# Performance work log

Measured on AMD Instinct MI355X. Metric: run time of the kernel, lower is better.

Reference implementation:

```python
import jax, jax.numpy as jnp
import numpy as np

CTX_SIZE = 4096
LAYER = 1
N_EMBD = 1024
HEAD_SIZE = 64
B, T = 4, 4096


def setup_inputs() -> dict:
    key = jax.random.key(0)
    ks = jax.random.split(key, 4)
    s = 1.0 / np.sqrt(N_EMBD)
    return {
        "x": jax.random.normal(ks[0], (B, T, N_EMBD), dtype=jnp.float32),
        "Wq": jax.random.normal(ks[1], (N_EMBD, HEAD_SIZE), dtype=jnp.float32) * s,
        "bq": jnp.zeros((HEAD_SIZE,), dtype=jnp.float32),
        "Wk": jax.random.normal(ks[2], (N_EMBD, HEAD_SIZE), dtype=jnp.float32) * s,
        "bk": jnp.zeros((HEAD_SIZE,), dtype=jnp.float32),
        "Wv": jax.random.normal(ks[3], (N_EMBD, HEAD_SIZE), dtype=jnp.float32) * s,
        "bv": jnp.zeros((HEAD_SIZE,), dtype=jnp.float32),
    }


def reference(x, Wq, bq, Wk, bk, Wv, bv):
    Bx, Tx, C = x.shape
    t = CTX_SIZE // (2 ** LAYER)
    cut = min(Tx, t)  # static: shapes are concrete under jit

    k = x @ Wk + bk                      # [B, T, H]
    q = x[:, -cut:, :] @ Wq + bq         # [B, cut, H] (fade: queries on last cut tokens)
    v = x @ Wv + bv                      # [B, T, H]

    att = jnp.einsum("bqh,bkh->bqk", q, k) * (C ** -0.5)  # [B, cut, T]

    # row i corresponds to absolute query position (T - cut + i); causal: key j <= that pos
    q_pos = jnp.arange(cut) + (Tx - cut)   # [cut]
    k_pos = jnp.arange(Tx)                 # [T]
    mask = k_pos[None, :] <= q_pos[:, None]  # [cut, T], True = keep
    att = jnp.where(mask[None, :, :], att, -jnp.inf)
    att = jax.nn.softmax(att, axis=-1)
    # dropout p=0.0 (eval mode): identity

    out = jnp.einsum("bqk,bkh->bqh", att, v)  # [B, cut, H]
    return out
```

## Files before the change

### kernel.cpp

```cpp
#include <hip/hip_runtime.h>

#define BB 4
#define TT 4096
#define CUT 2048
#define CE 1024
#define HD 64
#define QSC 0.045084220027780106f

typedef unsigned short u16;
typedef unsigned int u32;
typedef __attribute__((ext_vector_type(8))) short bf16x8;
typedef __attribute__((ext_vector_type(4))) float f32x4;

__device__ __forceinline__ u16 f2b(float f) {
  union { float f; unsigned u; } v; v.f = f;
  unsigned r = v.u + 0x7fffu + ((v.u >> 16) & 1u);
  return (u16)(r >> 16);
}

__device__ __forceinline__ u32 cvtpk(float lo, float hi) {
  u32 r;
  asm("v_cvt_pk_bf16_f32 %0, %1, %2" : "=v"(r) : "v"(lo), "v"(hi));
  return r;
}

__global__ void wtrans_k(const float* __restrict__ Wk, const float* __restrict__ Wv,
                         const float* __restrict__ Wq, u16* __restrict__ w3f) {
  int id = blockIdx.x * 256 + threadIdx.x;
  int j    = id & 7;
  int lane = (id >> 3) & 63;
  int f    = id >> 9;
  int kstep = f & 31;
  int mnt   = f >> 5;
  int m  = mnt >> 2;
  int nt = mnt & 3;
  int k   = kstep * 32 + (lane >> 4) * 8 + j;
  int col = nt * 16 + (lane & 15);
  const float* W = (m == 0) ? Wk : (m == 1) ? Wv : Wq;
  w3f[id] = f2b(W[k * 64 + col]);
}

__launch_bounds__(256, 2)
__global__ void proj_k(const float* __restrict__ x, const u16* __restrict__ w3f,
                       const float* __restrict__ bk, const float* __restrict__ bv,
                       const float* __restrict__ bq,
                       u16* __restrict__ KF, u16* __restrict__ VF, u16* __restrict__ Qb) {
  __shared__ f32x4 cl[2][2][12][64];
  const int tid  = threadIdx.x;
  const int lane = tid & 63;
  const int kh   = tid >> 6;
  const int l15  = lane & 15;
  const int g    = lane >> 4;
  const int r0   = blockIdx.x * 32;

  f32x4 acc[2][12];
  #pragma unroll
  for (int h = 0; h < 2; ++h)
    #pragma unroll
    for (int t = 0; t < 12; ++t) acc[h][t] = (f32x4){0.f, 0.f, 0.f, 0.f};

  const float* x0 = x + (size_t)(r0 + l15) * CE;
  const float* x1 = x + (size_t)(r0 + 16 + l15) * CE;

  f32x4 xs[2][4];
  {
    const int ko = kh * 256 + g * 8;
    xs[0][0] = *(const f32x4*)(x0 + ko);
    xs[0][1] = *(const f32x4*)(x0 + ko + 4);
    xs[0][2] = *(const f32x4*)(x1 + ko);
    xs[0][3] = *(const f32x4*)(x1 + ko + 4);
  }

  #pragma unroll
  for (int kc = 0; kc < 8; ++kc) {
    const int cur = kc & 1, nxt = cur ^ 1;
    if (kc < 7) {
      const int ko = kh * 256 + (kc + 1) * 32 + g * 8;
      xs[nxt][0] = *(const f32x4*)(x0 + ko);
      xs[nxt][1] = *(const f32x4*)(x0 + ko + 4);
      xs[nxt][2] = *(const f32x4*)(x1 + ko);
      xs[nxt][3] = *(const f32x4*)(x1 + ko + 4);
    }
    bf16x8 a0, a1;
    #pragma unroll
    for (int j = 0; j < 4; ++j) {
      a0[j] = (short)f2b(xs[cur][0][j]); a0[j + 4] = (short)f2b(xs[cur][1][j]);
      a1[j] = (short)f2b(xs[cur][2][j]); a1[j + 4] = (short)f2b(xs[cur][3][j]);
    }
    const int kstep = kh * 8 + kc;
    #pragma unroll
    for (int mnt = 0; mnt < 12; ++mnt) {
      bf16x8 bfr = *(const bf16x8*)&w3f[(size_t)(mnt * 32 + kstep) * 512 + lane * 8];
      acc[0][mnt] = __builtin_amdgcn_mfma_f32_16x16x32_bf16(a0, bfr, acc[0][mnt], 0, 0, 0);
      acc[1][mnt] = __builtin_amdgcn_mfma_f32_16x16x32_bf16(a1, bfr, acc[1][mnt], 0, 0, 0);
    }
  }

  if (kh >= 2) {
    #pragma unroll
    for (int h = 0; h < 2; ++h)
      #pragma unroll
      for (int t = 0; t < 12; ++t) cl[kh - 2][h][t][lane] = acc[h][t];
  }
  __syncthreads();
  if (kh < 2) {
    #pragma unroll
    for (int h = 0; h < 2; ++h)
      #pragma unroll
      for (int t = 0; t < 12; ++t) acc[h][t] += cl[kh][h][t][lane];
  }
  __syncthreads();
  if (kh == 1) {
    #pragma unroll
    for (int h = 0; h < 2; ++h)
      #pragma unroll
      for (int t = 0; t < 12; ++t) cl[0][h][t][lane] = acc[h][t];
  }
  __syncthreads();
  if (kh == 0) {
    #pragma unroll
    for (int h = 0; h < 2; ++h)
      #pragma unroll
      for (int t = 0; t < 12; ++t) acc[h][t] += cl[0][h][t][lane];
    #pragma unroll
    for (int h = 0; h < 2; ++h)
      #pragma unroll
      for (int t = 0; t < 8; ++t) cl[1][h][t][lane] = acc[h][t];
  }
  __syncthreads();

  const int b    = r0 >> 12;
  const int cch  = (r0 >> 6) & 63;
  const int half = (r0 >> 5) & 1;

  if (kh == 0) {
    const int t0 = r0 & (TT - 1);
    if (t0 >= CUT) {
      const int trow = t0 - CUT;
      #pragma unroll
      for (int h = 0; h < 2; ++h)
        #pragma unroll
        for (int nt = 0; nt < 4; ++nt) {
          int col = nt * 16 + l15;
          float bc = bq[col];
          #pragma unroll
          for (int r = 0; r < 4; ++r) {
            int qrow = trow + h * 16 + g * 4 + r;
            Qb[((size_t)b * CUT + qrow) * HD + col] = f2b((acc[h][8 + nt][r] + bc) * QSC);
          }
        }
    }
  } else if (kh == 1) {
    u16* KFc = KF + ((size_t)(b * 64 + cch) * 8) * 512;
    #pragma unroll
    for (int h = 0; h < 2; ++h) {
      const int kt2 = (half * 2 + h) * 2;
      #pragma unroll
      for (int nt = 0; nt < 4; ++nt) {
        int col = nt * 16 + l15;
        float bc = bk[col];
        f32x4 v = cl[1][h][nt][lane];
        const int off = (kt2 + (nt >> 1)) * 512 + 128 * ((nt & 1) * 2 + (l15 >> 3)) + (l15 & 7);
        #pragma unroll
        for (int r = 0; r < 4; ++r)
          KFc[off + (g * 4 + r) * 8] = f2b(v[r] + bc);
      }
    }
  } else if (kh == 2) {
    u16* VFc = VF + ((size_t)(b * 64 + cch) * 8) * 512;
    #pragma unroll
    for (int h = 0; h < 2; ++h) {
      #pragma unroll
      for (int nt = 0; nt < 4; ++nt) {
        int col = nt * 16 + l15;
        float bc = bv[col];
        f32x4 v = cl[1][h][4 + nt][lane];
        #pragma unroll
        for (int r = 0; r < 4; ++r) {
          int tt = h * 16 + g * 4 + r;
          VFc[(half * 4 + nt) * 512 + (l15 + 16 * (tt >> 3)) * 8 + (tt & 7)] = f2b(v[r] + bc);
        }
      }
    }
  }
}

__launch_bounds__(512, 4)
__global__ void attn_k(const u16* __restrict__ Qb, const u16* __restrict__ KF,
                       const u16* __restrict__ VF, float* __restrict__ out) {
  __shared__ u32   PLd[8][16][36];
  __shared__ float OO[8][16][66];
  __shared__ float OL[8][16];
  const int tid  = threadIdx.x;
  const int lane = tid & 63;
  const int wv   = tid >> 6;
  const int l15  = lane & 15;
  const int g    = lane >> 4;
  const int id   = blockIdx.x;
  const int b    = id & 3;
  const int i0   = (id >> 2) * 16;

  const int qabs = CUT + i0 + l15;
  const int qmin = CUT + i0;

  const u16* qrow = Qb + ((size_t)b * CUT + i0 + l15) * HD;
  bf16x8 qf0 = *(const bf16x8*)&qrow[g * 8];
  bf16x8 qf1 = *(const bf16x8*)&qrow[32 + g * 8];

  f32x4 o[4];
  #pragma unroll
  for (int dt = 0; dt < 4; ++dt) o[dt] = (f32x4){0.f, 0.f, 0.f, 0.f};
  float lsum = 0.f;

  const int kv_end = CUT + i0 + 16;
  const int nch = (kv_end + 63) >> 6;
  const u16* KFb = KF + (size_t)b * 64 * 8 * 512;
  const u16* VFb = VF + (size_t)b * 64 * 8 * 512;

  for (int c = wv; c < nch; c += 8) {
    const int kv0 = c << 6;

    const u16* kp = KFb + (size_t)c * 4096 + lane * 8;
    bf16x8 ka[4][2];
    #pragma unroll
    for (int kt = 0; kt < 4; ++kt) {
      ka[kt][0] = *(const bf16x8*)(kp + (kt * 2 + 0) * 512);
      ka[kt][1] = *(const bf16x8*)(kp + (kt * 2 + 1) * 512);
    }
    const u16* vp = VFb + (size_t)c * 4096 + lane * 8;
    bf16x8 va[2][4];
    #pragma unroll
    for (int c2 = 0; c2 < 2; ++c2)
      #pragma unroll
      for (int dt = 0; dt < 4; ++dt)
        va[c2][dt] = *(const bf16x8*)(vp + (c2 * 4 + dt) * 512);

    f32x4 st[4];
    __builtin_amdgcn_s_setprio(1);
    #pragma unroll
    for (int kt = 0; kt < 4; ++kt) {
      f32x4 s = (f32x4){0.f, 0.f, 0.f, 0.f};
      s = __builtin_amdgcn_mfma_f32_16x16x32_bf16(ka[kt][0], qf0, s, 0, 0, 0);
      s = __builtin_amdgcn_mfma_f32_16x16x32_bf16(ka[kt][1], qf1, s, 0, 0, 0);
      st[kt] = s;
    }
    __builtin_amdgcn_s_setprio(0);

    if (kv0 + 63 <= qmin) {
      #pragma unroll
      for (int kt = 0; kt < 4; ++kt)
        #pragma unroll
        for (int r = 0; r < 4; ++r) {
          float p = exp2f(st[kt][r]);
          st[kt][r] = p;
          lsum += p;
        }
    } else {
      #pragma unroll
      for (int kt = 0; kt < 4; ++kt)
        #pragma unroll
        for (int r = 0; r < 4; ++r) {
          int key = kv0 + kt * 16 + g * 4 + r;
          float p = exp2f(st[kt][r]);
          p = (key <= qabs) ? p : 0.f;
          st[kt][r] = p;
          lsum += p;
        }
    }

    #pragma unroll
    for (int kt = 0; kt < 4; ++kt) {
      u32 d0 = cvtpk(st[kt][0], st[kt][1]);
      u32 d1 = cvtpk(st[kt][2], st[kt][3]);
      u32* p = &PLd[wv][l15][kt * 8 + g * 2];
      p[0] = d0; p[1] = d1;
    }

    __builtin_amdgcn_s_setprio(1);
    #pragma unroll
    for (int c2 = 0; c2 < 2; ++c2) {
      bf16x8 pa = *(const bf16x8*)&PLd[wv][l15][c2 * 16 + g * 4];
      #pragma unroll
      for (int dt = 0; dt < 4; ++dt)
        o[dt] = __builtin_amdgcn_mfma_f32_16x16x32_bf16(pa, va[c2][dt], o[dt], 0, 0, 0);
    }
    __builtin_amdgcn_s_setprio(0);
  }

  lsum += __shfl_xor(lsum, 16);
  lsum += __shfl_xor(lsum, 32);
  if (lane < 16) OL[wv][l15] = lsum;
  #pragma unroll
  for (int dt = 0; dt < 4; ++dt)
    #pragma unroll
    for (int r = 0; r < 4; ++r)
      OO[wv][g * 4 + r][dt * 16 + l15] = o[dt][r];
  __syncthreads();

  #pragma unroll
  for (int e = tid; e < 1024; e += 512) {
    int q = e >> 6, d = e & 63;
    float L = 0.f, O = 0.f;
    #pragma unroll
    for (int w = 0; w < 8; ++w) { L += OL[w][q]; O += OO[w][q][d]; }
    out[((size_t)b * CUT + i0 + q) * HD + d] = O / L;
  }
}

extern "C" void kernel_launch(void* const* d_in, const int* in_sizes, int n_in,
                              void* d_out, int out_size, void* d_ws, size_t ws_size,
                              hipStream_t stream) {
  const float* x  = (const float*)d_in[0];
  const float* Wq = (const float*)d_in[1];
  const float* bq = (const float*)d_in[2];
  const float* Wk = (const float*)d_in[3];
  const float* bk = (const float*)d_in[4];
  const float* Wv = (const float*)d_in[5];
  const float* bv = (const float*)d_in[6];
  float* out = (float*)d_out;

  u16* Qb  = (u16*)d_ws;
  u16* W3F = Qb + (size_t)BB * CUT * HD;
  u16* KF  = W3F + (size_t)384 * 512;
  u16* VF  = KF + (size_t)BB * 64 * 8 * 512;

  wtrans_k<<<768, 256, 0, stream>>>(Wk, Wv, Wq, W3F);
  proj_k<<<512, 256, 0, stream>>>(x, W3F, bk, bv, bq, KF, VF, Qb);
  attn_k<<<512, 512, 0, stream>>>(Qb, KF, VF, out);
}
```

Before: 53.41 us.

## Stage projection weights in LDS via global_load_lds and split waves by row group

The projection kernel now stages the bf16 weight fragments into double-buffered shared memory with direct global-to-LDS loads, instead of each wave reading them from global memory. Waves are re-split so each handles one 16-row group and half of the K dimension, which cuts the cross-wave reduction from four partial sums to two. The aim is less redundant global weight traffic and a cheaper reduction. In exchange it adds a full vmcnt wait and a barrier on every K step, which may serialize loads and compute.

```diff
diff --git a/kernel.cpp b/kernel.cpp
--- a/kernel.cpp
+++ b/kernel.cpp
@@ -22,6 +22,11 @@
   u32 r;
   asm("v_cvt_pk_bf16_f32 %0, %1, %2" : "=v"(r) : "v"(lo), "v"(hi));
   return r;
+}
+
+__device__ __forceinline__ void gld16(const u16* g, u16* l) {
+  __builtin_amdgcn_global_load_lds((const __attribute__((address_space(1))) u32*)g,
+                                   (__attribute__((address_space(3))) u32*)l, 16, 0, 0);
 }
 
 __global__ void wtrans_k(const float* __restrict__ Wk, const float* __restrict__ Wv,
@@ -45,136 +50,114 @@
                        const float* __restrict__ bk, const float* __restrict__ bv,
                        const float* __restrict__ bq,
                        u16* __restrict__ KF, u16* __restrict__ VF, u16* __restrict__ Qb) {
-  __shared__ f32x4 cl[2][2][12][64];
+  __shared__ u16  st[2][2][12][512];
+  __shared__ f32x4 cl[2][12][64];
   const int tid  = threadIdx.x;
   const int lane = tid & 63;
-  const int kh   = tid >> 6;
+  const int wv   = tid >> 6;
+  const int rg   = wv & 1;
+  const int kh   = wv >> 1;
   const int l15  = lane & 15;
   const int g    = lane >> 4;
   const int r0   = blockIdx.x * 32;
 
-  f32x4 acc[2][12];
-  #pragma unroll
-  for (int h = 0; h < 2; ++h)
-    #pragma unroll
-    for (int t = 0; t < 12; ++t) acc[h][t] = (f32x4){0.f, 0.f, 0.f, 0.f};
-
-  const float* x0 = x + (size_t)(r0 + l15) * CE;
-  const float* x1 = x + (size_t)(r0 + 16 + l15) * CE;
-
-  f32x4 xs[2][4];
-  {
-    const int ko = kh * 256 + g * 8;
-    xs[0][0] = *(const f32x4*)(x0 + ko);
-    xs[0][1] = *(const f32x4*)(x0 + ko + 4);
-    xs[0][2] = *(const f32x4*)(x1 + ko);
-    xs[0][3] = *(const f32x4*)(x1 + ko + 4);
-  }
-
-  #pragma unroll
-  for (int kc = 0; kc < 8; ++kc) {
-    const int cur = kc & 1, nxt = cur ^ 1;
-    if (kc < 7) {
-      const int ko = kh * 256 + (kc + 1) * 32 + g * 8;
-      xs[nxt][0] = *(const f32x4*)(x0 + ko);
-      xs[nxt][1] = *(const f32x4*)(x0 + ko + 4);
-      xs[nxt][2] = *(const f32x4*)(x1 + ko);
-      xs[nxt][3] = *(const f32x4*)(x1 + ko + 4);
-    }
-    bf16x8 a0, a1;
+  f32x4 acc[12];
+  #pragma unroll
+  for (int t = 0; t < 12; ++t) acc[t] = (f32x4){0.f, 0.f, 0.f, 0.f};
+
+  const float* xrow = x + (size_t)(r0 + rg * 16 + l15) * CE + kh * 512;
+
+  #define STAGE(buf, t)                                                        \
+    {                                                                          \
+      _Pragma("unroll")                                                        \
+      for (int i = 0; i < 6; ++i) {                                            \
+        int jj = wv * 6 + i;                                                   \
+        int hh = jj / 12, mm = jj % 12;                                        \
+        gld16(&w3f[(size_t)(mm * 32 + hh * 16 + (t)) * 512 + lane * 8],        \
+              &st[buf][hh][mm][0]);                                            \
+      }                                                                        \
+    }
+
+  f32x4 xs[2][2];
+  xs[0][0] = *(const f32x4*)(xrow + g * 8);
+  xs[0][1] = *(const f32x4*)(xrow + g * 8 + 4);
+  STAGE(0, 0);
+  asm volatile("s_waitcnt vmcnt(0)" ::: "memory");
+  __syncthreads();
+
+  #pragma unroll
+  for (int t = 0; t < 16; ++t) {
+    const int cur = t & 1, nxt = cur ^ 1;
+    if (t < 15) {
+      STAGE(nxt, t + 1);
+      const float* xp = xrow + (t + 1) * 32 + g * 8;
+      xs[nxt][0] = *(const f32x4*)xp;
+      xs[nxt][1] = *(const f32x4*)(xp + 4);
+    }
+    bf16x8 a;
     #pragma unroll
     for (int j = 0; j < 4; ++j) {
-      a0[j] = (short)f2b(xs[cur][0][j]); a0[j + 4] = (short)f2b(xs[cur][1][j]);
-      a1[j] = (short)f2b(xs[cur][2][j]); a1[j + 4] = (short)f2b(xs[cur][3][j]);
-    }
-    const int kstep = kh * 8 + kc;
+      a[j]     = (short)f2b(xs[cur][0][j]);
+      a[j + 4] = (short)f2b(xs[cur][1][j]);
+    }
     #pragma unroll
     for (int mnt = 0; mnt < 12; ++mnt) {
-      bf16x8 bfr = *(const bf16x8*)&w3f[(size_t)(mnt * 32 + kstep) * 512 + lane * 8];
-      acc[0][mnt] = __builtin_amdgcn_mfma_f32_16x16x32_bf16(a0, bfr, acc[0][mnt], 0, 0, 0);
-      acc[1][mnt] = __builtin_amdgcn_mfma_f32_16x16x32_bf16(a1, bfr, acc[1][mnt], 0, 0, 0);
-    }
-  }
-
-  if (kh >= 2) {
-    #pragma unroll
-    for (int h = 0; h < 2; ++h)
-      #pragma unroll
-      for (int t = 0; t < 12; ++t) cl[kh - 2][h][t][lane] = acc[h][t];
-  }
-  __syncthreads();
-  if (kh < 2) {
-    #pragma unroll
-    for (int h = 0; h < 2; ++h)
-      #pragma unroll
-      for (int t = 0; t < 12; ++t) acc[h][t] += cl[kh][h][t][lane];
-  }
-  __syncthreads();
+      bf16x8 bfr = *(const bf16x8*)&st[cur][kh][mnt][lane * 8];
+      acc[mnt] = __builtin_amdgcn_mfma_f32_16x16x32_bf16(a, bfr, acc[mnt], 0, 0, 0);
+    }
+    asm volatile("s_waitcnt vmcnt(0)" ::: "memory");
+    __syncthreads();
+  }
+  #undef STAGE
+
   if (kh == 1) {
     #pragma unroll
-    for (int h = 0; h < 2; ++h)
-      #pragma unroll
-      for (int t = 0; t < 12; ++t) cl[0][h][t][lane] = acc[h][t];
+    for (int t = 0; t < 12; ++t) cl[rg][t][lane] = acc[t];
   }
   __syncthreads();
   if (kh == 0) {
     #pragma unroll
-    for (int h = 0; h < 2; ++h)
-      #pragma unroll
-      for (int t = 0; t < 12; ++t) acc[h][t] += cl[0][h][t][lane];
-    #pragma unroll
-    for (int h = 0; h < 2; ++h)
-      #pragma unroll
-      for (int t = 0; t < 8; ++t) cl[1][h][t][lane] = acc[h][t];
-  }
-  __syncthreads();
-
-  const int b    = r0 >> 12;
-  const int cch  = (r0 >> 6) & 63;
-  const int half = (r0 >> 5) & 1;
-
-  if (kh == 0) {
+    for (int t = 0; t < 12; ++t) acc[t] += cl[rg][t][lane];
+
+    const int b    = r0 >> 12;
+    const int cch  = (r0 >> 6) & 63;
+    const int half = (r0 >> 5) & 1;
+    const int h    = rg;
+
     const int t0 = r0 & (TT - 1);
     if (t0 >= CUT) {
-      const int trow = t0 - CUT;
-      #pragma unroll
-      for (int h = 0; h < 2; ++h)
-        #pragma unroll
-        for (int nt = 0; nt < 4; ++nt) {
-          int col = nt * 16 + l15;
-          float bc = bq[col];
-          #pragma unroll
-          for (int r = 0; r < 4; ++r) {
-            int qrow = trow + h * 16 + g * 4 + r;
-            Qb[((size_t)b * CUT + qrow) * HD + col] = f2b((acc[h][8 + nt][r] + bc) * QSC);
-          }
-        }
-    }
-  } else if (kh == 1) {
-    u16* KFc = KF + ((size_t)(b * 64 + cch) * 8) * 512;
-    #pragma unroll
-    for (int h = 0; h < 2; ++h) {
+      const int trow = t0 - CUT + h * 16;
+      #pragma unroll
+      for (int nt = 0; nt < 4; ++nt) {
+        int col = nt * 16 + l15;
+        float bc = bq[col];
+        #pragma unroll
+        for (int r = 0; r < 4; ++r)
+          Qb[((size_t)b * CUT + trow + g * 4 + r) * HD + col] =
+              f2b((acc[8 + nt][r] + bc) * QSC);
+      }
+    }
+    {
+      u16* KFc = KF + ((size_t)(b * 64 + cch) * 8) * 512;
       const int kt2 = (half * 2 + h) * 2;
       #pragma unroll
       for (int nt = 0; nt < 4; ++nt) {
         int col = nt * 16 + l15;
         float bc = bk[col];
-        f32x4 v = cl[1][h][nt][lane];
+        f32x4 v = acc[nt];
         const int off = (kt2 + (nt >> 1)) * 512 + 128 * ((nt & 1) * 2 + (l15 >> 3)) + (l15 & 7);
         #pragma unroll
         for (int r = 0; r < 4; ++r)
           KFc[off + (g * 4 + r) * 8] = f2b(v[r] + bc);
       }
     }
-  } else if (kh == 2) {
-    u16* VFc = VF + ((size_t)(b * 64 + cch) * 8) * 512;
-    #pragma unroll
-    for (int h = 0; h < 2; ++h) {
+    {
+      u16* VFc = VF + ((size_t)(b * 64 + cch) * 8) * 512;
       #pragma unroll
       for (int nt = 0; nt < 4; ++nt) {
         int col = nt * 16 + l15;
         float bc = bv[col];
-        f32x4 v = cl[1][h][4 + nt][lane];
+        f32x4 v = acc[4 + nt];
         #pragma unroll
         for (int r = 0; r < 4; ++r) {
           int tt = h * 16 + g * 4 + r;
```

Result: faster. 50.15 us (-6.1%).
